# Performance work log

Measured on AMD Instinct MI355X. Metric: run time of the kernel, lower is better.

## Reference

```python
import jax, jax.numpy as jnp
import numpy as np

# CODABlocks (codomain attention) with per_channel_attention=True:
# token_codimension = head_codimension = 1, scale = 2, n_modes = [32, 32],
# mixer_modes = [16, 16], temperature = 1.0, instance_norm (affine) everywhere.
N_HEADS = 16
TEMPERATURE = 1.0
EPS = 1e-5

def _gelu(z):
    return jax.nn.gelu(z, approximate=False)  # matches torch F.gelu default (erf)

def instance_norm(x, g, b):
    # x: (B, C, H, W); normalize over spatial dims per (sample, channel), affine.
    mu = jnp.mean(x, axis=(-2, -1), keepdims=True)
    var = jnp.var(x, axis=(-2, -1), keepdims=True)
    return (x - mu) * jax.lax.rsqrt(var + EPS) * g[:, None, None] + b[:, None, None]

def conv1x1(x, w, b):
    return jnp.einsum('bihw,io->bohw', x, w) + b[None, :, None, None]

def fourier_resample(x, out_shape):
    # FFT-based spatial resampling (mode truncation / zero-pad), norm='forward'.
    if tuple(x.shape[-2:]) == tuple(out_shape):
        return x
    Ho, Wo = out_shape
    xft = jnp.fft.rfftn(x, axes=(-2, -1), norm='forward')
    out = jnp.zeros(x.shape[:-2] + (Ho, Wo // 2 + 1), dtype=xft.dtype)
    hk = min(x.shape[-2], Ho) // 2
    wk = min(xft.shape[-1], Wo // 2 + 1)
    out = out.at[..., :hk, :wk].set(xft[..., :hk, :wk])
    out = out.at[..., -hk:, :wk].set(xft[..., -hk:, :wk])
    return jnp.fft.irfftn(out, s=out_shape, axes=(-2, -1), norm='forward')

def spectral_conv(x, w, out_shape):
    # Truncated-mode spectral convolution (dense weights, equiv. to tucker rank=1.0).
    # w: (Cin, Cout, 2*mh, mw, 2) -> complex weight on kept Fourier modes.
    wc = w[..., 0] + 1j * w[..., 1]
    mh = wc.shape[2] // 2
    mw = wc.shape[3]
    Ho, Wo = out_shape
    xft = jnp.fft.rfftn(x, axes=(-2, -1), norm='forward')   # (B, Cin, H, W//2+1)
    top = jnp.einsum('bihw,iohw->bohw', xft[:, :, :mh, :mw], wc[:, :, :mh])
    bot = jnp.einsum('bihw,iohw->bohw', xft[:, :, -mh:, :mw], wc[:, :, mh:])
    out_ft = jnp.zeros((x.shape[0], wc.shape[1], Ho, Wo // 2 + 1), dtype=xft.dtype)
    out_ft = out_ft.at[:, :, :mh, :mw].set(top)
    out_ft = out_ft.at[:, :, -mh:, :mw].set(bot)
    return jnp.fft.irfftn(out_ft, s=out_shape, axes=(-2, -1), norm='forward')

def fno_layer(x, spec_w, skip_w, skip_b, out_shape, norm=None, act=None):
    # One FNOBlocks layer: spectral conv + (resampled) linear skip, optional norm/act.
    xs = fourier_resample(conv1x1(x, skip_w, skip_b), out_shape)
    xf = spectral_conv(x, spec_w, out_shape)
    if norm is not None:
        xf = instance_norm(xf, *norm)
    y = xf + xs
    return act(y) if act is not None else y

def codano_forward(x, key_w, key_skip_w, key_skip_b, query_w, query_skip_w, query_skip_b, value_w, value_skip_w, value_skip_b, proj_w, proj_skip_w, proj_skip_b, norm1_g, norm1_b, attn_norm_g, attn_norm_b, norm2_g, norm2_b, mixer_w1, mixer_skip_w1, mixer_skip_b1, mixer_norm_g1, mixer_norm_b1, mixer_w2, mixer_skip_w2, mixer_skip_b2, mixer_norm_g2, mixer_norm_b2, mixer_out_g, mixer_out_b):
    b, t, H, W = x.shape   # token codim d = 1 -> channel dim == number of tokens
    tokens = x.reshape(b * t, 1, H, W)
    tokens_norm = instance_norm(tokens, norm1_g, norm1_b)
    Hs, Ws = H // 2, W // 2   # K, Q downsampled by scale = 2
    k = fno_layer(tokens_norm, key_w, key_skip_w, key_skip_b, (Hs, Ws))
    q = fno_layer(tokens_norm, query_w, query_skip_w, query_skip_b, (Hs, Ws))
    v = fno_layer(tokens_norm, value_w, value_skip_w, value_skip_b, (H, W))

    def heads_flat(z):
        hh, ww = z.shape[-2:]
        # (b*t, n_heads*d, h, w) -> (b, heads, t, d*h*w), d = 1
        return z.reshape(b, t, N_HEADS, hh * ww).transpose(0, 2, 1, 3)

    kf, qf, vf = heads_flat(k), heads_flat(q), heads_flat(v)
    scale = jnp.sqrt(jnp.asarray(kf.shape[-1], jnp.float32)) * TEMPERATURE
    dprod = jax.nn.softmax(jnp.einsum('bhtd,bhsd->bhts', qf, kf) / scale, axis=-1)
    attn = jnp.einsum('bhts,bhsd->bhtd', dprod, vf)      # (b, heads, t, H*W)
    attn = attn.transpose(0, 2, 1, 3).reshape(b * t, N_HEADS, H, W)
    # multi-head projection back to token codimension (n_heads -> 1)
    attn = fno_layer(attn, proj_w, proj_skip_w, proj_skip_b, (H, W))
    attn = instance_norm(attn + tokens, attn_norm_g, attn_norm_b)
    # permutation-equivariant mixer: 2 FNO layers shared across all tokens
    m = instance_norm(attn, norm2_g, norm2_b)
    m = fno_layer(m, mixer_w1, mixer_skip_w1, mixer_skip_b1, (H, W), norm=(mixer_norm_g1, mixer_norm_b1), act=_gelu)
    m = fno_layer(m, mixer_w2, mixer_skip_w2, mixer_skip_b2, (H, W), norm=(mixer_norm_g2, mixer_norm_b2))
    out = instance_norm(m, mixer_out_g, mixer_out_b) + attn
    return out.reshape(b, t, H, W)

def setup_inputs():
    key = jax.random.key(0)
    ks = list(jax.random.split(key, 32))
    f32 = jnp.float32
    def W_(k, shape, s=0.02):
        return (s * jax.random.normal(k, shape)).astype(f32)
    B, T, H, Wd = 4, 32, 128, 128
    mh_s, mw_s = 16, 9    # mixer_modes [16,16]: 2*(16//2) rows, 16//2+1 rfft cols
    mh_f, mw_f = 32, 17   # n_modes [32,32]
    return {
        'x': jax.random.normal(ks[0], (B, T, H, Wd), dtype=f32),
        'key_w': W_(ks[1], (1, N_HEADS, mh_s, mw_s, 2)),
        'key_skip_w': W_(ks[2], (1, N_HEADS), 0.5),
        'key_skip_b': W_(ks[3], (N_HEADS,)),
        'query_w': W_(ks[4], (1, N_HEADS, mh_s, mw_s, 2)),
        'query_skip_w': W_(ks[5], (1, N_HEADS), 0.5),
        'query_skip_b': W_(ks[6], (N_HEADS,)),
        'value_w': W_(ks[7], (1, N_HEADS, mh_s, mw_s, 2)),
        'value_skip_w': W_(ks[8], (1, N_HEADS), 0.5),
        'value_skip_b': W_(ks[9], (N_HEADS,)),
        'proj_w': W_(ks[10], (N_HEADS, 1, mh_f, mw_f, 2)),
        'proj_skip_w': W_(ks[11], (N_HEADS, 1), 0.25),
        'proj_skip_b': W_(ks[12], (1,)),
        'norm1_g': jnp.ones((1,), f32), 'norm1_b': jnp.zeros((1,), f32),
        'attn_norm_g': jnp.ones((1,), f32), 'attn_norm_b': jnp.zeros((1,), f32),
        'norm2_g': jnp.ones((1,), f32), 'norm2_b': jnp.zeros((1,), f32),
        'mixer_w1': W_(ks[13], (1, 1, mh_f, mw_f, 2)),
        'mixer_skip_w1': W_(ks[14], (1, 1), 0.5),
        'mixer_skip_b1': W_(ks[15], (1,)),
        'mixer_norm_g1': jnp.ones((1,), f32), 'mixer_norm_b1': jnp.zeros((1,), f32),
        'mixer_w2': W_(ks[16], (1, 1, mh_f, mw_f, 2)),
        'mixer_skip_w2': W_(ks[17], (1, 1), 0.5),
        'mixer_skip_b2': W_(ks[18], (1,)),
        'mixer_norm_g2': jnp.ones((1,), f32), 'mixer_norm_b2': jnp.zeros((1,), f32),
        'mixer_out_g': jnp.ones((1,), f32), 'mixer_out_b': jnp.zeros((1,), f32),
    }

def reference(x, key_w, key_skip_w, key_skip_b, query_w, query_skip_w, query_skip_b, value_w, value_skip_w, value_skip_b, proj_w, proj_skip_w, proj_skip_b, norm1_g, norm1_b, attn_norm_g, attn_norm_b, norm2_g, norm2_b, mixer_w1, mixer_skip_w1, mixer_skip_b1, mixer_norm_g1, mixer_norm_b1, mixer_w2, mixer_skip_w2, mixer_skip_b2, mixer_norm_g2, mixer_norm_b2, mixer_out_g, mixer_out_b):
    return codano_forward(x, key_w, key_skip_w, key_skip_b, query_w, query_skip_w, query_skip_b, value_w, value_skip_w, value_skip_b, proj_w, proj_skip_w, proj_skip_b, norm1_g, norm1_b, attn_norm_g, attn_norm_b, norm2_g, norm2_b, mixer_w1, mixer_skip_w1, mixer_skip_b1, mixer_norm_g1, mixer_norm_b1, mixer_w2, mixer_skip_w2, mixer_skip_b2, mixer_norm_g2, mixer_norm_b2, mixer_out_g, mixer_out_b)
```

## Files before the change

### kernel.cpp

```cpp
#include <hip/hip_runtime.h>
#include <cmath>

#define PI_F 3.14159265358979323846f
#define NTOK 128
#define NPIX 16384
#define NHEADS 16

__device__ __forceinline__ void block_reduce2(float& a, float& b){
  __shared__ float sa[4], sb[4];
  __syncthreads();
  for (int o=32;o>0;o>>=1){ a += __shfl_down(a,o); b += __shfl_down(b,o); }
  int w = threadIdx.x>>6, l = threadIdx.x&63;
  if (l==0){ sa[w]=a; sb[w]=b; }
  __syncthreads();
  a = sa[0]+sa[1]+sa[2]+sa[3];
  b = sb[0]+sb[1]+sb[2]+sb[3];
}

__device__ __forceinline__ float block_reduce1(float a){
  __shared__ float sa[4];
  __syncthreads();
  for (int o=32;o>0;o>>=1) a += __shfl_down(a,o);
  int w = threadIdx.x>>6, l = threadIdx.x&63;
  if (l==0) sa[w]=a;
  __syncthreads();
  return sa[0]+sa[1]+sa[2]+sa[3];
}

__device__ __forceinline__ float gelu_f(float y){
  return 0.5f*y*(1.f + erff(y*0.70710678118f));
}

__device__ __forceinline__ void affine_from(const float* __restrict__ ps, float g, float bb, int t,
                                            float& a, float& b0){
  float sum=0.f,sq=0.f;
  #pragma unroll
  for (int s=0;s<8;s++){ const float* p=ps+((size_t)t*8+s)*2; sum+=p[0]; sq+=p[1]; }
  const float iN=1.f/NPIX;
  float mu=sum*iN, var=sq*iN-mu*mu;
  a=rsqrtf(var+1e-5f)*g;
  b0=bb-mu*a;
}
__device__ __forceinline__ void scalA_from(const float* __restrict__ psA, float ag, float n2g, int t,
                                           float& muZ, float& aA, float& a0){
  float sum=0.f,sq=0.f;
  #pragma unroll
  for (int s=0;s<16;s++){ const float* p=psA+((size_t)t*16+s)*2; sum+=p[0]; sq+=p[1]; }
  const float iN=1.f/NPIX;
  muZ=sum*iN; float var=sq*iN-muZ*muZ;
  float inv=rsqrtf(var+1e-5f);
  aA=inv*ag;
  float var2=aA*aA*var;
  a0=aA*rsqrtf(var2+1e-5f)*n2g;
}
__device__ __forceinline__ void scalB_from(const float* __restrict__ psB, float mng1, int t,
                                           float& mu1, float& c1){
  float sum=0.f,sq=0.f;
  #pragma unroll
  for (int s=0;s<16;s++){ const float* p=psB+((size_t)t*16+s)*2; sum+=p[0]; sq+=p[1]; }
  const float iN=1.f/NPIX;
  mu1=sum*iN; float var=sq*iN-mu1*mu1;
  c1=rsqrtf(var+1e-5f)*mng1;
}
__device__ __forceinline__ void scalC_from(const float* __restrict__ psC, float mng2, float K, float sw,
                                           float outg, int t,
                                           float& mu2f, float& c2, float& mu3, float& c3){
  float sf=0.f,sfsq=0.f,sm=0.f,smsq=0.f,sx=0.f;
  #pragma unroll
  for (int s=0;s<16;s++){
    const float* p=psC+((size_t)t*16+s)*5;
    sf+=p[0]; sfsq+=p[1]; sm+=p[2]; smsq+=p[3]; sx+=p[4];
  }
  const float iN=1.f/NPIX;
  mu2f=sf*iN; float var2=sfsq*iN-mu2f*mu2f;
  c2=rsqrtf(var2+1e-5f)*mng2;
  float Em1=sm*iN, Em1sq=smsq*iN, Exm=sx*iN;
  float Em2=K+sw*Em1;
  float Em2sq = c2*c2*var2 + sw*sw*Em1sq + K*K
              + 2.f*c2*sw*(Exm - mu2f*Em1) + 2.f*K*sw*Em1;
  float var_m2=Em2sq-Em2*Em2;
  mu3=Em2;
  c3=rsqrtf(var_m2+1e-5f)*outg;
}

__global__ __launch_bounds__(256) void k_stats0(const float* __restrict__ x, float* __restrict__ pstat){
  int t=blockIdx.x, slab=blockIdx.y;
  const float* xs = x + (size_t)t*NPIX + slab*2048;
  float sum=0.f, sq=0.f;
  for (int i=threadIdx.x;i<2048;i+=256){ float v=xs[i]; sum+=v; sq+=v*v; }
  block_reduce2(sum,sq);
  if (threadIdx.x==0){ float* o=pstat+((size_t)t*8+slab)*2; o[0]=sum; o[1]=sq; }
}

__global__ __launch_bounds__(256) void k_colfft33(const float* __restrict__ x, const float* __restrict__ pstat0,
                          const float* __restrict__ n1g, const float* __restrict__ n1b,
                          float* __restrict__ A){
  __shared__ float rows[16*128];
  __shared__ float tw[128][2];
  int base = blockIdx.x*16;
  int t = base>>7;
  float a,b0; affine_from(pstat0, n1g[0], n1b[0], t, a, b0);
  for (int i=threadIdx.x;i<2048;i+=256) rows[i] = a*x[(size_t)base*128 + i] + b0;
  for (int p=threadIdx.x;p<128;p+=256){ float sn,cs; sincosf(-(2.f*PI_F/128.f)*(float)p,&sn,&cs); tw[p][0]=cs; tw[p][1]=sn; }
  __syncthreads();
  for (int e=threadIdx.x;e<16*33;e+=256){
    int r=e/33, c=e%33;
    const float* rp=rows+r*128;
    float re=0.f, im=0.f;
    for (int w=0;w<128;w++){
      int p=(c*w)&127;
      float v=rp[w];
      re+=v*tw[p][0]; im+=v*tw[p][1];
    }
    float* o=A+((size_t)(base+r)*33+c)*2; o[0]=re; o[1]=im;
  }
}

__global__ __launch_bounds__(256) void k_rowfft64(const float* __restrict__ A,
                          float* __restrict__ X64, float* __restrict__ X64h){
  int s=blockIdx.x, cg=blockIdx.y;
  int c0=cg*11;
  __shared__ float a[128][11][2];
  __shared__ float S[64][11][2];
  __shared__ float tw[128][2];
  for (int i=threadIdx.x;i<128*22;i+=256){
    int r=i/22, q=i%22;
    a[r][q>>1][q&1] = A[((size_t)(s*128+r)*33 + c0)*2 + q];
  }
  for (int p=threadIdx.x;p<128;p+=256){ float sn,cs; sincosf(-(2.f*PI_F/128.f)*(float)p,&sn,&cs); tw[p][0]=cs; tw[p][1]=sn; }
  __syncthreads();
  const float sc=1.f/16384.f;
  for (int e=threadIdx.x;e<64*11;e+=256){
    int i2=e/11, cl=e%11;
    int r=(i2<32)? i2 : i2+64;
    float re=0.f, im=0.f;
    for (int h=0;h<128;h++){
      int p=(r*h)&127;
      float cs=tw[p][0], sn=tw[p][1];
      float ar=a[h][cl][0], ai=a[h][cl][1];
      re+=ar*cs-ai*sn; im+=ar*sn+ai*cs;
    }
    S[i2][cl][0]=re*sc; S[i2][cl][1]=im*sc;
  }
  __syncthreads();
  for (int e=threadIdx.x;e<64*11;e+=256){
    int r=e/11, cl=e%11; int c=c0+cl;
    float vr=S[r][cl][0], vi=S[r][cl][1];
    float* o=X64+((size_t)s*(64*33)+r*33+c)*2; o[0]=vr; o[1]=vi;
    float hr=vr, hi=vi;
    if (c==0 || c==32){
      int pr=(64-r)&63;
      hr=0.5f*(vr+S[pr][cl][0]);
      hi=0.5f*(vi-S[pr][cl][1]);
    }
    float* oh=X64h+((size_t)s*(64*33)+r*33+c)*2; oh[0]=hr; oh[1]=hi;
  }
}

__global__ __launch_bounds__(256) void k_UeZYw(const float* __restrict__ X64, const float* __restrict__ X64h,
    const float* __restrict__ qw, const float* __restrict__ qsw,
    const float* __restrict__ kw, const float* __restrict__ ksw,
    const float* __restrict__ value_w, const float* __restrict__ vsw, const float* __restrict__ vsb,
    const float* __restrict__ proj_w, const float* __restrict__ psw,
    float* __restrict__ Zq, float* __restrict__ Zk, float* __restrict__ Yw,
    float* __restrict__ Ue){
  __shared__ float sh[4224];
  int bx=blockIdx.x;
  if (bx<2048){
    int t=bx>>4, h=bx&15;
    float* Xs = sh;
    float2* xh0 = (float2*)(sh+1092);
    for (int e=threadIdx.x;e<544;e+=256){
      int j=e/17, c=e%17;
      int i2=(j<16)? j : (j+32);
      const float* xp = X64 + ((size_t)t*(64*33) + i2*33 + c)*2;
      Xs[e*2]=xp[0]; Xs[e*2+1]=xp[1];
    }
    if (threadIdx.x<17){
      int j=threadIdx.x;
      int r=(j<=8)? j : j+47;
      const float* hp = X64h + ((size_t)t*(64*33) + r*33)*2;
      xh0[j]=make_float2(hp[0],hp[1]);
    }
    __syncthreads();
    float aq=qsw[h], ak=ksw[h];
    for (int e=threadIdx.x;e<306;e+=256){
      int side=e/153, m=e%153;
      int j=m/9, c=m%9;
      int jj=(j<=8)? j : j+15;
      const float* W = side? kw : qw;
      float a = side? ak : aq;
      float prx=0.f, pry=0.f;
      if (j!=8){
        int jw=(j<8)? j : j-1;
        const float* wp = W + ((size_t)(h*16+jw)*9 + c)*2;
        float xrr=Xs[(jj*17+c)*2], xri=Xs[(jj*17+c)*2+1];
        prx = wp[0]*xrr - wp[1]*xri;
        pry = wp[0]*xri + wp[1]*xrr;
      }
      float Vx=prx, Vy=pry;
      if (c==0){
        int jp = (j==0)? 0 : 17-j;
        float ppx=0.f, ppy=0.f;
        if (jp!=8){
// ... 137 lines not shown
    int e0=ec*64, hs0=g*128;
    float (*Pl)[32] = (float(*)[32])sh;
    for (int i=threadIdx.x;i<128*32;i+=256){
      int hsl=i>>5, t=i&31;
      int hs=hs0+hsl, h=hs>>5, s=hs&31;
      Pl[hsl][t]=P[(((size_t)(b*16+h)*32)+t)*32+s];
    }
    __syncthreads();
    int el=threadIdx.x&63, tg=threadIdx.x>>6;
    float acc[8];
    #pragma unroll
    for (int j=0;j<8;j++) acc[j]=0.f;
    const float* Yb = Yw + ((size_t)b*512 + hs0)*1088 + e0 + el;
    #pragma unroll 4
    for (int hsl=0;hsl<128;hsl++){
      float y = Yb[(size_t)hsl*1088];
      #pragma unroll
      for (int j=0;j<8;j++) acc[j] += Pl[hsl][tg*8+j]*y;
    }
    #pragma unroll
    for (int j=0;j<8;j++){
      int t=tg*8+j;
      Sfp[((size_t)(b*32+t)*4+g)*1088 + e0 + el] = acc[j];
    }
  } else {
    int u=bx-272;
    int b=u>>6, rem=u&63, ch=rem>>1, tt=rem&1;
    int pxb=ch*512;
    float* Rs = sh;
    float* cbs = sh+512;
    float* as2 = sh+528;
    float* b0s = sh+560;
    if (threadIdx.x<32){
      float a,b0; affine_from(pstat0, n1g[0], n1b[0], b*32+threadIdx.x, a, b0);
      as2[threadIdx.x]=a; b0s[threadIdx.x]=b0;
    }
    __syncthreads();
    for (int rr=threadIdx.x; rr<512; rr+=256){
      int tl=rr>>5, s=rr&31;
      int t=tt*16+tl;
      float acc=0.f;
      for (int h=0;h<16;h++)
        acc += pw[h]*vw[h]*P[(((size_t)(b*16+h)*32)+t)*32+s];
      Rs[tl*32+s]=acc*as2[s];
      float cb=acc*b0s[s];
      for (int o=16;o>0;o>>=1) cb+=__shfl_down(cb,o,32);
      if (s==0) cbs[tl]=cb;
    }
    __syncthreads();
    float a0[16], a1[16];
    #pragma unroll
    for (int t=0;t<16;t++){ a0[t]=0.f; a1[t]=0.f; }
    for (int s=0;s<32;s++){
      const float* xp = x + ((size_t)(b*32+s))*NPIX + pxb;
      float v0=xp[threadIdx.x], v1=xp[threadIdx.x+256];
      #pragma unroll
      for (int t=0;t<16;t++){ float r=Rs[t*32+s]; a0[t]+=r*v0; a1[t]+=r*v1; }
    }
    #pragma unroll
    for (int t=0;t<16;t++){
      int gt=tt*16+t;
      float cb=cbs[t];
      float* op = sk + ((size_t)(b*32+gt))*NPIX + pxb;
      op[threadIdx.x]=a0[t]+cb; op[threadIdx.x+256]=a1[t]+cb;
    }
  }
}

__global__ __launch_bounds__(256) void k_field0(const float* __restrict__ Sfp,
        const float* __restrict__ sk, const float* __restrict__ x,
        const float* __restrict__ psw, const float* __restrict__ vsb, const float* __restrict__ psb,
        float* __restrict__ zf, float* __restrict__ pstatA){
  int bt = blockIdx.x, slab = blockIdx.y;
  __shared__ float Ss[1088];
  __shared__ float T[8*17*2];
  __shared__ float tw[128][2];
  for (int i=threadIdx.x;i<1088;i+=256){
    const float* sp4 = Sfp + (size_t)bt*4352 + i;
    Ss[i] = sp4[0]+sp4[1088]+sp4[2176]+sp4[3264];
  }
  for (int p=threadIdx.x;p<128;p+=256){ float sn,cs; sincosf((2.f*PI_F/128.f)*(float)p,&sn,&cs); tw[p][0]=cs; tw[p][1]=sn; }
  __syncthreads();
  int h0 = slab*8;
  for (int e=threadIdx.x;e<8*17;e+=256){
    int hl=e/17, c=e%17; int h=h0+hl;
    float re=0.f, im=0.f;
    for (int j=0;j<32;j++){
      int r=(j<16)? j : (j+96);
      int p=(r*h)&127;
      float cs=tw[p][0], sn=tw[p][1];
      float ar=Ss[(j*17+c)*2], ai=Ss[(j*17+c)*2+1];
      re += ar*cs - ai*sn;
      im += ar*sn + ai*cs;
    }
    T[e*2]=re; T[e*2+1]=im;
  }
  __syncthreads();
  size_t base = (size_t)bt*NPIX + h0*128;
  float Cb = psb[0];
  for (int hh=0;hh<16;hh++) Cb += psw[hh]*vsb[hh];
  float sum=0.f, sq=0.f;
  for (int pos=threadIdx.x;pos<1024;pos+=256){
    int hl=pos>>7, w=pos&127;
    const float* Th=T+hl*17*2;
    float br=tw[w][0], bi=tw[w][1];
    float rr=br, ri=bi;
    float v=Th[0];
    for (int c=1;c<17;c++){
      v += 2.f*(Th[c*2]*rr - Th[c*2+1]*ri);
      float nr=rr*br-ri*bi; ri=rr*bi+ri*br; rr=nr;
    }
    float val = v + sk[base+pos] + x[base+pos] + Cb;
    zf[base+pos]=val; sum+=val; sq+=val*val;
  }
  block_reduce2(sum,sq);
  if (threadIdx.x==0){ float* o=pstatA+((size_t)bt*16+slab)*2; o[0]=sum; o[1]=sq; }
}

__global__ __launch_bounds__(256) void k_specm0(const float* __restrict__ P,
    const float* __restrict__ pw, const float* __restrict__ vw,
    const float* __restrict__ Sfp, const float* __restrict__ X64,
    const float* __restrict__ pstat0, const float* __restrict__ pstatA,
    const float* __restrict__ n1g, const float* __restrict__ n1b,
    const float* __restrict__ ag, const float* __restrict__ n2g, const float* __restrict__ n2b,
    const float* __restrict__ psw, const float* __restrict__ vsb, const float* __restrict__ psb,
    float* __restrict__ sp){
  int bt=blockIdx.x, ec=blockIdx.y; int b=bt>>5, t=bt&31;
  __shared__ float Rs[32];
  __shared__ float Sfl[1088];
  if (threadIdx.x<32){
    int s=threadIdx.x; float acc=0.f;
    for (int h=0;h<16;h++)
      acc += pw[h]*vw[h]*P[(((size_t)(b*16+h)*32)+t)*32+s];
    Rs[s]=acc;
  }
  for (int i=threadIdx.x;i<1088;i+=256){
    const float* sp4 = Sfp + (size_t)bt*4352 + i;
    Sfl[i]=sp4[0]+sp4[1088]+sp4[2176]+sp4[3264];
  }
  __syncthreads();
  float a_t,b0_t; affine_from(pstat0,n1g[0],n1b[0],bt,a_t,b0_t);
  float muZ,aA,a0; scalA_from(pstatA,ag[0],n2g[0],bt,muZ,aA,a0);
  float Cb=psb[0];
  for (int h=0;h<16;h++) Cb+=psw[h]*vsb[h];
  float inva=1.f/a_t;
  int e1=ec*272, e2=e1+272;
  for (int e=e1+threadIdx.x;e<e2;e+=256){
    int j=e/17, c=e%17;
    float sr=Sfl[e*2], si=Sfl[e*2+1];
    if (c==0){
      if (j==0){ si=0.f; }
      else if (j==16){ sr*=0.5f; si*=0.5f; }
      else { int jp=32-j; sr=0.5f*(sr+Sfl[jp*34]); si=0.5f*(si-Sfl[jp*34+1]); }
    }
    int i2=(j<16)? j : (j+32);
    float re=0.f, im=0.f;
    const float* xb = X64 + ((size_t)(b*32)*(64*33) + i2*33 + c)*2;
    for (int s=0;s<32;s++){
      const float* xp = xb + (size_t)s*(64*33)*2;
      float r=Rs[s];
      re += r*xp[0]; im += r*xp[1];
    }
    const float* xt = X64 + ((size_t)bt*(64*33) + i2*33 + c)*2;
    re += inva*xt[0]; im += inva*xt[1];
    float zr=sr+re, zi=si+im;
    if (e==0) zr += Cb - b0_t*inva;
    float mr=a0*zr, mi=a0*zi;
    if (e==0) mr += n2b[0] - muZ*a0;
    sp[((size_t)bt*544+e)*2]=mr; sp[((size_t)bt*544+e)*2+1]=mi;
  }
}

__global__ __launch_bounds__(256) void k_field1(const float* __restrict__ sp, const float* __restrict__ wm,
        float* __restrict__ fd1, float* __restrict__ pstatB){
  int bt = blockIdx.x, slab = blockIdx.y;
  __shared__ float Ss[1088];
  __shared__ float T[8*17*2];
  __shared__ float tw[128][2];
  for (int e=threadIdx.x;e<544;e+=256){
    float xr=sp[((size_t)bt*544+e)*2], xi=sp[((size_t)bt*544+e)*2+1];
    float wr=wm[e*2], wi=wm[e*2+1];
    Ss[e*2]=xr*wr-xi*wi; Ss[e*2+1]=xr*wi+xi*wr;
  }
  for (int p=threadIdx.x;p<128;p+=256){ float sn,cs; sincosf((2.f*PI_F/128.f)*(float)p,&sn,&cs); tw[p][0]=cs; tw[p][1]=sn; }
  __syncthreads();
  int h0 = slab*8;
  for (int e=threadIdx.x;e<8*17;e+=256){
    int hl=e/17, c=e%17; int h=h0+hl;
    float re=0.f, im=0.f;
    for (int j=0;j<32;j++){
      int r=(j<16)? j : (j+96);
      int p=(r*h)&127;
      float cs=tw[p][0], sn=tw[p][1];
      float ar=Ss[(j*17+c)*2], ai=Ss[(j*17+c)*2+1];
      re += ar*cs - ai*sn;
      im += ar*sn + ai*cs;
    }
    T[e*2]=re; T[e*2+1]=im;
  }
  __syncthreads();
  size_t base = (size_t)bt*NPIX + h0*128;
  float sum=0.f, sq=0.f;
  for (int pos=threadIdx.x;pos<1024;pos+=256){
    int hl=pos>>7, w=pos&127;
    const float* Th=T+hl*17*2;
    float br=tw[w][0], bi=tw[w][1];
    float rr=br, ri=bi;
    float v=Th[0];
    for (int c=1;c<17;c++){
      v += 2.f*(Th[c*2]*rr - Th[c*2+1]*ri);
      float nr=rr*br-ri*bi; ri=rr*bi+ri*br; rr=nr;
    }
    fd1[base+pos]=v; sum+=v; sq+=v*v;
  }
  block_reduce2(sum,sq);
  if (threadIdx.x==0){ float* o=pstatB+((size_t)bt*16+slab)*2; o[0]=sum; o[1]=sq; }
}

__global__ __launch_bounds__(256) void k_colA1(const float* __restrict__ f1, const float* __restrict__ z,
        const float* __restrict__ pstatA, const float* __restrict__ pstatB,
        const float* __restrict__ ag, const float* __restrict__ n2g, const float* __restrict__ mng1,
        const float* __restrict__ n2b,
        const float* __restrict__ mnb1, const float* __restrict__ msw1, const float* __restrict__ msb1,
        float* __restrict__ A){
  __shared__ float rows[16*128];
  __shared__ float tw[128][2];
  int grow = blockIdx.x*16;
  int t = grow>>7;
  float muZ,aA,a0;
  scalA_from(pstatA, ag[0], n2g[0], t, muZ, aA, a0);
  float b2 = n2b[0];
  float mu1,c1;
  scalB_from(pstatB, mng1[0], t, mu1, c1);
  float nb=mnb1[0], sw=msw1[0], sb=msb1[0];
  for (int i=threadIdx.x;i<2048;i+=256){
    size_t gi=(size_t)grow*128+i;
    float m0v=(z[gi]-muZ)*a0+b2;
    float y=(f1[gi]-mu1)*c1+nb + m0v*sw + sb;
    rows[i]=gelu_f(y);
  }
  for (int p=threadIdx.x;p<128;p+=256){ float sn,cs; sincosf(-(2.f*PI_F/128.f)*(float)p,&sn,&cs); tw[p][0]=cs; tw[p][1]=sn; }
  __syncthreads();
  for (int e=threadIdx.x;e<16*17;e+=256){
    int r=e/17, c=e%17;
    const float* rp=rows+r*128;
    float re=0.f, im=0.f;
    for (int w=0;w<128;w++){
      int p=(c*w)&127;
      float v=rp[w];
      re+=v*tw[p][0]; im+=v*tw[p][1];
    }
    float* o=A+((size_t)(grow+r)*17+c)*2; o[0]=re; o[1]=im;
  }
}

__global__ __launch_bounds__(256) void k_rowfft32(const float* __restrict__ A, float* __restrict__ spec){
  int s=blockIdx.x, cg=blockIdx.y;
  int c0 = (cg==0)? 0 : (1+cg*4);
  int nc = (cg==0)? 5 : 4;
  __shared__ float a[128*5*2];
  __shared__ float tw[128][2];
  for (int i=threadIdx.x;i<128*nc*2;i+=256){
    int r=i/(2*nc), q=i%(2*nc);
    a[(r*5+(q>>1))*2+(q&1)] = A[((size_t)(s*128+r)*17 + c0)*2 + q];
  }
  for (int p=threadIdx.x;p<128;p+=256){ float sn,cs; sincosf(-(2.f*PI_F/128.f)*(float)p,&sn,&cs); tw[p][0]=cs; tw[p][1]=sn; }
  __syncthreads();
  const float sc=1.f/16384.f;
  for (int e=threadIdx.x;e<32*nc;e+=256){
    int j=e/nc, cl=e%nc;
    int r=(j<16)? j : (j+96);
    float re=0.f,im=0.f;
    for (int h=0;h<128;h++){
      int p=(r*h)&127;
      float cs=tw[p][0], sn=tw[p][1];
      float ar=a[(h*5+cl)*2], ai=a[(h*5+cl)*2+1];
      re += ar*cs - ai*sn;
      im += ar*sn + ai*cs;
    }
    float* o=spec+((size_t)s*544 + j*17 + c0+cl)*2;
    o[0]=re*sc; o[1]=im*sc;
  }
}

__global__ __launch_bounds__(256) void k_field2(const float* __restrict__ sp2, const float* __restrict__ wm,
        const float* __restrict__ f1, const float* __restrict__ z,
        const float* __restrict__ pstatA, const float* __restrict__ pstatB,
        const float* __restrict__ ag, const float* __restrict__ n2g, const float* __restrict__ mng1,
        const float* __restrict__ n2b, const float* __restrict__ mnb1,
        const float* __restrict__ msw1, const float* __restrict__ msb1,
        float* __restrict__ fd2, float* __restrict__ pstatC){
  int bt = blockIdx.x, slab = blockIdx.y;
  __shared__ float Ss[1088];
  __shared__ float T[8*17*2];
  __shared__ float tw[128][2];
  for (int e=threadIdx.x;e<544;e+=256){
    float xr=sp2[((size_t)bt*544+e)*2], xi=sp2[((size_t)bt*544+e)*2+1];
    float wr=wm[e*2], wi=wm[e*2+1];
    Ss[e*2]=xr*wr-xi*wi; Ss[e*2+1]=xr*wi+xi*wr;
  }
  for (int p=threadIdx.x;p<128;p+=256){ float sn,cs; sincosf((2.f*PI_F/128.f)*(float)p,&sn,&cs); tw[p][0]=cs; tw[p][1]=sn; }
  __syncthreads();
  int h0 = slab*8;
  for (int e=threadIdx.x;e<8*17;e+=256){
    int hl=e/17, c=e%17; int h=h0+hl;
    float re=0.f, im=0.f;
    for (int j=0;j<32;j++){
      int r=(j<16)? j : (j+96);
      int p=(r*h)&127;
      float cs=tw[p][0], sn=tw[p][1];
      float ar=Ss[(j*17+c)*2], ai=Ss[(j*17+c)*2+1];
      re += ar*cs - ai*sn;
      im += ar*sn + ai*cs;
    }
    T[e*2]=re; T[e*2+1]=im;
  }
  __syncthreads();
  size_t base = (size_t)bt*NPIX + h0*128;
  float muZ,aA,a0,mu1,c1;
  scalA_from(pstatA, ag[0], n2g[0], bt, muZ, aA, a0);
  scalB_from(pstatB, mng1[0], bt, mu1, c1);
  float b2=n2b[0], nb1=mnb1[0], sw1=msw1[0], sb1=msb1[0];
  float s_f=0.f,s_fsq=0.f,s_m=0.f,s_msq=0.f,s_x=0.f;
  for (int pos=threadIdx.x;pos<1024;pos+=256){
    int hl=pos>>7, w=pos&127;
    const float* Th=T+hl*17*2;
    float br=tw[w][0], bi=tw[w][1];
    float rr=br, ri=bi;
    float v=Th[0];
    for (int c=1;c<17;c++){
      v += 2.f*(Th[c*2]*rr - Th[c*2+1]*ri);
      float nr=rr*br-ri*bi; ri=rr*bi+ri*br; rr=nr;
    }
    size_t gi=base+pos;
    float m0v=(z[gi]-muZ)*a0+b2;
    float y=(f1[gi]-mu1)*c1+nb1 + m0v*sw1 + sb1;
    float m1v=gelu_f(y);
    fd2[gi]=v;
    s_f+=v; s_fsq+=v*v; s_m+=m1v; s_msq+=m1v*m1v; s_x+=v*m1v;
  }
  block_reduce2(s_f,s_fsq);
  block_reduce2(s_m,s_msq);
  s_x = block_reduce1(s_x);
  if (threadIdx.x==0){
    float* o=pstatC+((size_t)bt*16+slab)*5;
    o[0]=s_f; o[1]=s_fsq; o[2]=s_m; o[3]=s_msq; o[4]=s_x;
  }
}

__global__ __launch_bounds__(256) void k_final2(const float* __restrict__ z, const float* __restrict__ f1,
        const float* __restrict__ f2,
        const float* __restrict__ pstatA, const float* __restrict__ pstatB, const float* __restrict__ pstatC,
        const float* __restrict__ ag, const float* __restrict__ n2g, const float* __restrict__ mng1,
        const float* __restrict__ mng2, const float* __restrict__ outg,
        const float* __restrict__ ab, const float* __restrict__ n2b,
        const float* __restrict__ mnb1, const float* __restrict__ msw1, const float* __restrict__ msb1,
        const float* __restrict__ mnb2, const float* __restrict__ msw2, const float* __restrict__ msb2,
        const float* __restrict__ outb, float* __restrict__ out){
  int bt=blockIdx.x, slab=blockIdx.y;
  float muZ,aA,a0,mu1,c1,mu2f,c2,mu3,c3;
  scalA_from(pstatA, ag[0], n2g[0], bt, muZ, aA, a0);
  scalB_from(pstatB, mng1[0], bt, mu1, c1);
  float sw2=msw2[0], K=mnb2[0]+msb2[0];
  scalC_from(pstatC, mng2[0], K, sw2, outg[0], bt, mu2f, c2, mu3, c3);
  float b1=ab[0], b2=n2b[0], nb1=mnb1[0], sw1=msw1[0], sb1=msb1[0];
  float nb2=mnb2[0], sb2=msb2[0], bo=outb[0];
  size_t base=(size_t)bt*NPIX + (size_t)slab*1024;
  for (int i=threadIdx.x;i<1024;i+=256){
    size_t gi=base+i;
    float zv=z[gi];
    float m0v=(zv-muZ)*a0+b2;
    float a2v=(zv-muZ)*aA+b1;
    float y=(f1[gi]-mu1)*c1+nb1 + m0v*sw1 + sb1;
    float m1v=gelu_f(y);
    float m2v=(f2[gi]-mu2f)*c2+nb2 + m1v*sw2 + sb2;
    out[gi]=(m2v-mu3)*c3+bo+a2v;
  }
}

extern "C" void kernel_launch(void* const* d_in, const int* in_sizes, int n_in,
                              void* d_out, int out_size, void* d_ws, size_t ws_size,
                              hipStream_t stream){
  const float* x        = (const float*)d_in[0];
  const float* key_w    = (const float*)d_in[1];
  const float* key_sw   = (const float*)d_in[2];
  const float* key_sb   = (const float*)d_in[3];
  const float* query_w  = (const float*)d_in[4];
  const float* query_sw = (const float*)d_in[5];
  const float* query_sb = (const float*)d_in[6];
  const float* value_w  = (const float*)d_in[7];
  const float* value_sw = (const float*)d_in[8];
  const float* value_sb = (const float*)d_in[9];
  const float* proj_w   = (const float*)d_in[10];
  const float* proj_sw  = (const float*)d_in[11];
  const float* proj_sb  = (const float*)d_in[12];
  const float* norm1_g  = (const float*)d_in[13];
  const float* norm1_b  = (const float*)d_in[14];
  const float* attn_g   = (const float*)d_in[15];
  const float* attn_b   = (const float*)d_in[16];
  const float* norm2_g  = (const float*)d_in[17];
  const float* norm2_b  = (const float*)d_in[18];
  const float* mw1      = (const float*)d_in[19];
  const float* msw1     = (const float*)d_in[20];
  const float* msb1     = (const float*)d_in[21];
  const float* mng1     = (const float*)d_in[22];
  const float* mnb1     = (const float*)d_in[23];
  const float* mw2      = (const float*)d_in[24];
  const float* msw2     = (const float*)d_in[25];
  const float* msb2     = (const float*)d_in[26];
  const float* mng2     = (const float*)d_in[27];
  const float* mnb2     = (const float*)d_in[28];
  const float* outg     = (const float*)d_in[29];
  const float* outb     = (const float*)d_in[30];
  float* out = (float*)d_out;
  float* ws  = (float*)d_ws;

  size_t off=0;
  float* A   = ws + off; off += (size_t)128*128*33*2;
  float* X64 = ws + off; off += (size_t)128*64*33*2;
  float* X64h= ws + off; off += (size_t)128*64*33*2;
  float* Zq  = ws + off; off += (size_t)128*16*306;
  float* Zk  = ws + off; off += (size_t)128*16*306;
  float* Ue  = ws + off; off += (size_t)4*32*32;
  float* P   = ws + off; off += (size_t)4*16*32*32;
  float* Yw  = ws + off; off += (size_t)2048*1088;
  float* Sfp = ws + off; off += (size_t)128*4*1088;
  float* sk  = ws + off; off += (size_t)128*16384;
  float* zf  = ws + off; off += (size_t)128*16384;
  float* fd1 = ws + off; off += (size_t)128*16384;
  float* fd2 = ws + off; off += (size_t)128*16384;
  float* sp  = ws + off; off += (size_t)128*544*2;
  float* sp2 = ws + off; off += (size_t)128*544*2;
  float* pstat0 = ws + off; off += (size_t)128*8*2;
  float* pstatA = ws + off; off += (size_t)128*16*2;
  float* pstatB = ws + off; off += (size_t)128*16*2;
  float* pstatC = ws + off; off += (size_t)128*16*5;

  k_stats0<<<dim3(128,8),256,0,stream>>>(x, pstat0);
  k_colfft33<<<1024,256,0,stream>>>(x, pstat0, norm1_g, norm1_b, A);
  k_rowfft64<<<dim3(128,3),256,0,stream>>>(A, X64, X64h);
  k_UeZYw<<<3072,256,0,stream>>>(X64, X64h, query_w, query_sw, key_w, key_sw,
      value_w, value_sw, value_sb, proj_w, proj_sw, Zq, Zk, Yw, Ue);
  k_scores2<<<dim3(4,16,2),256,0,stream>>>(Zq, Zk, Ue, query_sw, query_sb, key_sw, key_sb, P);
  k_SfSk<<<528,256,0,stream>>>(x, P, Yw, proj_sw, value_sw, pstat0, norm1_g, norm1_b, Sfp, sk);

  k_field0<<<dim3(128,16),256,0,stream>>>(Sfp, sk, x, proj_sw, value_sb, proj_sb, zf, pstatA);
  k_specm0<<<dim3(128,2),256,0,stream>>>(P, proj_sw, value_sw, Sfp, X64, pstat0, pstatA,
      norm1_g, norm1_b, attn_g, norm2_g, norm2_b, proj_sw, value_sb, proj_sb, sp);
  k_field1<<<dim3(128,16),256,0,stream>>>(sp, mw1, fd1, pstatB);
  k_colA1<<<1024,256,0,stream>>>(fd1, zf, pstatA, pstatB, attn_g, norm2_g, mng1,
      norm2_b, mnb1, msw1, msb1, A);
  k_rowfft32<<<dim3(128,4),256,0,stream>>>(A, sp2);
  k_field2<<<dim3(128,16),256,0,stream>>>(sp2, mw2, fd1, zf, pstatA, pstatB,
      attn_g, norm2_g, mng1, norm2_b, mnb1, msw1, msb1, fd2, pstatC);
  k_final2<<<dim3(128,16),256,0,stream>>>(zf, fd1, fd2, pstatA, pstatB, pstatC,
      attn_g, norm2_g, mng1, mng2, outg, attn_b, norm2_b,
      mnb1, msw1, msb1, mnb2, msw2, msb2, outb, out);
}
```

Baseline: 307.6 us.

## Fuse tail kernel chain into one cooperative persistent kernel with grid syncs

Replaces the seven tail launches (field0, specm0, field1, colA1, rowfft32, field2, final2) with one cooperative kernel of 512 blocks that loops over the same work units and separates the stages with grid-wide syncs. The aim is to remove per-launch overhead and the gaps between dependent small kernels. In exchange it adds grid barrier cost, caps parallelism at the resident grid, and falls back to the separate launches if the cooperative launch fails.

```diff
diff --git a/kernel.cpp b/kernel.cpp
--- a/kernel.cpp
+++ b/kernel.cpp
@@ -1,5 +1,8 @@
 #include <hip/hip_runtime.h>
+#include <hip/hip_cooperative_groups.h>
 #include <cmath>
+
+namespace cg = cooperative_groups;
 
 #define PI_F 3.14159265358979323846f
 #define NTOK 128
@@ -118,8 +121,8 @@
 
 __global__ __launch_bounds__(256) void k_rowfft64(const float* __restrict__ A,
                           float* __restrict__ X64, float* __restrict__ X64h){
-  int s=blockIdx.x, cg=blockIdx.y;
-  int c0=cg*11;
+  int s=blockIdx.x, cg2=blockIdx.y;
+  int c0=cg2*11;
   __shared__ float a[128][11][2];
   __shared__ float S[64][11][2];
   __shared__ float tw[128][2];
@@ -423,7 +426,7 @@
   for (int p=threadIdx.x;p<128;p+=256){ float sn,cs; sincosf((2.f*PI_F/128.f)*(float)p,&sn,&cs); tw[p][0]=cs; tw[p][1]=sn; }
   __syncthreads();
   int h0 = slab*8;
-  for (int e=threadIdx.x;e<8*17;e+=256){
+  for (int e=threadIdx.x;e<136;e+=256){
     int hl=e/17, c=e%17; int h=h0+hl;
     float re=0.f, im=0.f;
     for (int j=0;j<32;j++){
@@ -526,7 +529,7 @@
   for (int p=threadIdx.x;p<128;p+=256){ float sn,cs; sincosf((2.f*PI_F/128.f)*(float)p,&sn,&cs); tw[p][0]=cs; tw[p][1]=sn; }
   __syncthreads();
   int h0 = slab*8;
-  for (int e=threadIdx.x;e<8*17;e+=256){
+  for (int e=threadIdx.x;e<136;e+=256){
     int hl=e/17, c=e%17; int h=h0+hl;
     float re=0.f, im=0.f;
     for (int j=0;j<32;j++){
@@ -596,9 +599,9 @@
 }
 
 __global__ __launch_bounds__(256) void k_rowfft32(const float* __restrict__ A, float* __restrict__ spec){
-  int s=blockIdx.x, cg=blockIdx.y;
-  int c0 = (cg==0)? 0 : (1+cg*4);
-  int nc = (cg==0)? 5 : 4;
+  int s=blockIdx.x, cg2=blockIdx.y;
+  int c0 = (cg2==0)? 0 : (1+cg2*4);
+  int nc = (cg2==0)? 5 : 4;
   __shared__ float a[128*5*2];
   __shared__ float tw[128][2];
   for (int i=threadIdx.x;i<128*nc*2;i+=256){
@@ -643,7 +646,7 @@
   for (int p=threadIdx.x;p<128;p+=256){ float sn,cs; sincosf((2.f*PI_F/128.f)*(float)p,&sn,&cs); tw[p][0]=cs; tw[p][1]=sn; }
   __syncthreads();
   int h0 = slab*8;
-  for (int e=threadIdx.x;e<8*17;e+=256){
+  for (int e=threadIdx.x;e<136;e+=256){
     int hl=e/17, c=e%17; int h=h0+hl;
     float re=0.f, im=0.f;
     for (int j=0;j<32;j++){
@@ -716,6 +719,322 @@
     float m1v=gelu_f(y);
     float m2v=(f2[gi]-mu2f)*c2+nb2 + m1v*sw2 + sb2;
     out[gi]=(m2v-mu3)*c3+bo+a2v;
+  }
+}
+
+struct TailArgs {
+  const float *Sfp, *sk, *x, *P, *X64, *pstat0;
+  float *pstatA, *pstatB, *pstatC, *sp, *sp2, *A, *zf, *fd1, *fd2, *out;
+  const float *n1g,*n1b,*ag,*n2g,*n2b,*mng1,*mnb1,*msw1,*msb1,*mw1,*mw2;
+  const float *mng2,*mnb2,*msw2,*msb2,*outg,*outb,*ab,*psw,*vsb,*psb,*pw,*vw;
+};
+
+#define TAIL_GRID 512
+
+__global__ __launch_bounds__(256,2) void k_tail(TailArgs Aa){
+  cg::grid_group gg = cg::this_grid();
+  __shared__ float sh[2304];
+
+  {
+    float* tw = sh+1360;
+    for (int p=threadIdx.x;p<128;p+=256){ float sn,cs; sincosf((2.f*PI_F/128.f)*(float)p,&sn,&cs); tw[p*2]=cs; tw[p*2+1]=sn; }
+    float Cb = Aa.psb[0];
+    for (int hh=0;hh<16;hh++) Cb += Aa.psw[hh]*Aa.vsb[hh];
+    for (int u=blockIdx.x; u<2048; u+=TAIL_GRID){
+      int bt=u>>4, slab=u&15;
+      __syncthreads();
+      float* Ss=sh; float* T=sh+1088;
+      for (int i=threadIdx.x;i<1088;i+=256){
+        const float* sp4 = Aa.Sfp + (size_t)bt*4352 + i;
+        Ss[i] = sp4[0]+sp4[1088]+sp4[2176]+sp4[3264];
+      }
+      __syncthreads();
+      int h0 = slab*8;
+      for (int e=threadIdx.x;e<136;e+=256){
+        int hl=e/17, c=e%17; int h=h0+hl;
+        float re=0.f, im=0.f;
+        for (int j=0;j<32;j++){
+          int r=(j<16)? j : (j+96);
+          int p=(r*h)&127;
+          float cs=tw[p*2], sn=tw[p*2+1];
+          float ar=Ss[(j*17+c)*2], ai=Ss[(j*17+c)*2+1];
+          re += ar*cs - ai*sn;
+          im += ar*sn + ai*cs;
+        }
+        T[e*2]=re; T[e*2+1]=im;
+      }
+      __syncthreads();
+      size_t base = (size_t)bt*NPIX + h0*128;
+      float sum=0.f, sq=0.f;
+      for (int pos=threadIdx.x;pos<1024;pos+=256){
+        int hl=pos>>7, w=pos&127;
+        const float* Th=T+hl*17*2;
+        float br=tw[w*2], bi=tw[w*2+1];
+        float rr=br, ri=bi;
+        float v=Th[0];
+        for (int c=1;c<17;c++){
+          v += 2.f*(Th[c*2]*rr - Th[c*2+1]*ri);
+          float nr=rr*br-ri*bi; ri=rr*bi+ri*br; rr=nr;
+        }
+        float val = v + Aa.sk[base+pos] + Aa.x[base+pos] + Cb;
+        Aa.zf[base+pos]=val; sum+=val; sq+=val*val;
+      }
+      block_reduce2(sum,sq);
+      if (threadIdx.x==0){ float* o=Aa.pstatA+((size_t)bt*16+slab)*2; o[0]=sum; o[1]=sq; }
+    }
+  }
+  gg.sync();
+
+  {
+    for (int u=blockIdx.x; u<256; u+=TAIL_GRID){
+      int bt=u>>1, ec=u&1; int b=bt>>5, t=bt&31;
+      __syncthreads();
+      float* Sfl=sh; float* Rs=sh+1088;
+      if (threadIdx.x<32){
+        int s=threadIdx.x; float acc=0.f;
+        for (int h=0;h<16;h++)
+          acc += Aa.pw[h]*Aa.vw[h]*Aa.P[(((size_t)(b*16+h)*32)+t)*32+s];
+        Rs[s]=acc;
+      }
+      for (int i=threadIdx.x;i<1088;i+=256){
+        const float* sp4 = Aa.Sfp + (size_t)bt*4352 + i;
+        Sfl[i]=sp4[0]+sp4[1088]+sp4[2176]+sp4[3264];
+      }
+      __syncthreads();
+      float a_t,b0_t; affine_from(Aa.pstat0,Aa.n1g[0],Aa.n1b[0],bt,a_t,b0_t);
+      float muZ,aA,a0; scalA_from(Aa.pstatA,Aa.ag[0],Aa.n2g[0],bt,muZ,aA,a0);
+      float Cb=Aa.psb[0];
+      for (int h=0;h<16;h++) Cb+=Aa.psw[h]*Aa.vsb[h];
+      float inva=1.f/a_t;
+      int e1=ec*272, e2=e1+272;
+      for (int e=e1+threadIdx.x;e<e2;e+=256){
+        int j=e/17, c=e%17;
+        float sr=Sfl[e*2], si=Sfl[e*2+1];
+        if (c==0){
+          if (j==0){ si=0.f; }
+          else if (j==16){ sr*=0.5f; si*=0.5f; }
+          else { int jp=32-j; sr=0.5f*(sr+Sfl[jp*34]); si=0.5f*(si-Sfl[jp*34+1]); }
+        }
+        int i2=(j<16)? j : (j+32);
+        float re=0.f, im=0.f;
+        const float* xb = Aa.X64 + ((size_t)(b*32)*(64*33) + i2*33 + c)*2;
+        for (int s=0;s<32;s++){
+          const float* xp = xb + (size_t)s*(64*33)*2;
+          float r=Rs[s];
+          re += r*xp[0]; im += r*xp[1];
+        }
+        const float* xt = Aa.X64 + ((size_t)bt*(64*33) + i2*33 + c)*2;
+        re += inva*xt[0]; im += inva*xt[1];
+        float zr=sr+re, zi=si+im;
+        if (e==0) zr += Cb - b0_t*inva;
+        float mr=a0*zr, mi=a0*zi;
+        if (e==0) mr += Aa.n2b[0] - muZ*a0;
+        Aa.sp[((size_t)bt*544+e)*2]=mr; Aa.sp[((size_t)bt*544+e)*2+1]=mi;
+      }
+    }
+  }
+  gg.sync();
+
+  {
+    float* tw = sh+1360;
+    for (int p=threadIdx.x;p<128;p+=256){ float sn,cs; sincosf((2.f*PI_F/128.f)*(float)p,&sn,&cs); tw[p*2]=cs; tw[p*2+1]=sn; }
+    for (int u=blockIdx.x; u<2048; u+=TAIL_GRID){
+      int bt=u>>4, slab=u&15;
+      __syncthreads();
+      float* Ss=sh; float* T=sh+1088;
+      for (int e=threadIdx.x;e<544;e+=256){
+        float xr=Aa.sp[((size_t)bt*544+e)*2], xi=Aa.sp[((size_t)bt*544+e)*2+1];
+        float wr=Aa.mw1[e*2], wi=Aa.mw1[e*2+1];
+        Ss[e*2]=xr*wr-xi*wi; Ss[e*2+1]=xr*wi+xi*wr;
+      }
+      __syncthreads();
+      int h0 = slab*8;
+      for (int e=threadIdx.x;e<136;e+=256){
+        int hl=e/17, c=e%17; int h=h0+hl;
+        float re=0.f, im=0.f;
+        for (int j=0;j<32;j++){
+          int r=(j<16)? j : (j+96);
+          int p=(r*h)&127;
+          float cs=tw[p*2], sn=tw[p*2+1];
+          float ar=Ss[(j*17+c)*2], ai=Ss[(j*17+c)*2+1];
+          re += ar*cs - ai*sn;
+          im += ar*sn + ai*cs;
+        }
+        T[e*2]=re; T[e*2+1]=im;
+      }
+      __syncthreads();
+      size_t base = (size_t)bt*NPIX + h0*128;
+      float sum=0.f, sq=0.f;
+      for (int pos=threadIdx.x;pos<1024;pos+=256){
+        int hl=pos>>7, w=pos&127;
+        const float* Th=T+hl*17*2;
+        float br=tw[w*2], bi=tw[w*2+1];
+        float rr=br, ri=bi;
+        float v=Th[0];
+        for (int c=1;c<17;c++){
+          v += 2.f*(Th[c*2]*rr - Th[c*2+1]*ri);
+          float nr=rr*br-ri*bi; ri=rr*bi+ri*br; rr=nr;
+        }
+        Aa.fd1[base+pos]=v; sum+=v; sq+=v*v;
+      }
+      block_reduce2(sum,sq);
+      if (threadIdx.x==0){ float* o=Aa.pstatB+((size_t)bt*16+slab)*2; o[0]=sum; o[1]=sq; }
+    }
+  }
+  gg.sync();
+
+  {
+    float* tw = sh+2048;
+    for (int p=threadIdx.x;p<128;p+=256){ float sn,cs; sincosf(-(2.f*PI_F/128.f)*(float)p,&sn,&cs); tw[p*2]=cs; tw[p*2+1]=sn; }
+    for (int u=blockIdx.x; u<1024; u+=TAIL_GRID){
+      int grow=u*16; int t=grow>>7;
+      __syncthreads();
+      float* rows=sh;
+      float muZ,aA,a0;
+      scalA_from(Aa.pstatA, Aa.ag[0], Aa.n2g[0], t, muZ, aA, a0);
+      float b2 = Aa.n2b[0];
+      float mu1,c1;
+      scalB_from(Aa.pstatB, Aa.mng1[0], t, mu1, c1);
+      float nb=Aa.mnb1[0], sw=Aa.msw1[0], sb=Aa.msb1[0];
+      for (int i=threadIdx.x;i<2048;i+=256){
+        size_t gi=(size_t)grow*128+i;
+        float m0v=(Aa.zf[gi]-muZ)*a0+b2;
+        float y=(Aa.fd1[gi]-mu1)*c1+nb + m0v*sw + sb;
+        rows[i]=gelu_f(y);
+      }
+      __syncthreads();
+      for (int e=threadIdx.x;e<16*17;e+=256){
+        int r=e/17, c=e%17;
+        const float* rp=rows+r*128;
+        float re=0.f, im=0.f;
+        for (int w=0;w<128;w++){
+          int p=(c*w)&127;
+          float v=rp[w];
+          re+=v*tw[p*2]; im+=v*tw[p*2+1];
+        }
+        float* o=Aa.A+((size_t)(grow+r)*17+c)*2; o[0]=re; o[1]=im;
+      }
+    }
+  }
+  gg.sync();
+
+  {
+    float* tw = sh+2048;
+    for (int p=threadIdx.x;p<128;p+=256){ float sn,cs; sincosf(-(2.f*PI_F/128.f)*(float)p,&sn,&cs); tw[p*2]=cs; tw[p*2+1]=sn; }
+    const float sc=1.f/16384.f;
+    for (int u=blockIdx.x; u<512; u+=TAIL_GRID){
+      int s=u>>2, cg2=u&3;
+      int c0 = (cg2==0)? 0 : (1+cg2*4);
+      int nc = (cg2==0)? 5 : 4;
+      __syncthreads();
+      float* a=sh;
+      for (int i=threadIdx.x;i<128*nc*2;i+=256){
+        int r=i/(2*nc), q=i%(2*nc);
+        a[(r*5+(q>>1))*2+(q&1)] = Aa.A[((size_t)(s*128+r)*17 + c0)*2 + q];
+      }
+      __syncthreads();
+      for (int e=threadIdx.x;e<32*nc;e+=256){
+        int j=e/nc, cl=e%nc;
+        int r=(j<16)? j : (j+96);
+        float re=0.f,im=0.f;
+        for (int h=0;h<128;h++){
+          int p=(r*h)&127;
+          float cs=tw[p*2], sn=tw[p*2+1];
+          float ar=a[(h*5+cl)*2], ai=a[(h*5+cl)*2+1];
+          re += ar*cs - ai*sn;
+          im += ar*sn + ai*cs;
+        }
+        float* o=Aa.sp2+((size_t)s*544 + j*17 + c0+cl)*2;
+        o[0]=re*sc; o[1]=im*sc;
+      }
+    }
+  }
+  gg.sync();
+
+  {
+    float* tw = sh+1360;
+    for (int p=threadIdx.x;p<128;p+=256){ float sn,cs; sincosf((2.f*PI_F/128.f)*(float)p,&sn,&cs); tw[p*2]=cs; tw[p*2+1]=sn; }
+    for (int u=blockIdx.x; u<2048; u+=TAIL_GRID){
+      int bt=u>>4, slab=u&15;
+      __syncthreads();
+      float* Ss=sh; float* T=sh+1088;
+      for (int e=threadIdx.x;e<544;e+=256){
+        float xr=Aa.sp2[((size_t)bt*544+e)*2], xi=Aa.sp2[((size_t)bt*544+e)*2+1];
+        float wr=Aa.mw2[e*2], wi=Aa.mw2[e*2+1];
+        Ss[e*2]=xr*wr-xi*wi; Ss[e*2+1]=xr*wi+xi*wr;
+      }
+      __syncthreads();
+      int h0 = slab*8;
+      for (int e=threadIdx.x;e<136;e+=256){
+        int hl=e/17, c=e%17; int h=h0+hl;
+        float re=0.f, im=0.f;
+        for (int j=0;j<32;j++){
+          int r=(j<16)? j : (j+96);
+          int p=(r*h)&127;
+          float cs=tw[p*2], sn=tw[p*2+1];
+          float ar=Ss[(j*17+c)*2], ai=Ss[(j*17+c)*2+1];
+          re += ar*cs - ai*sn;
+          im += ar*sn + ai*cs;
+        }
+        T[e*2]=re; T[e*2+1]=im;
+      }
+      __syncthreads();
+      size_t base = (size_t)bt*NPIX + h0*128;
+      float muZ,aA,a0,mu1,c1;
+      scalA_from(Aa.pstatA, Aa.ag[0], Aa.n2g[0], bt, muZ, aA, a0);
+      scalB_from(Aa.pstatB, Aa.mng1[0], bt, mu1, c1);
+      float b2=Aa.n2b[0], nb1=Aa.mnb1[0], sw1=Aa.msw1[0], sb1=Aa.msb1[0];
+      float s_f=0.f,s_fsq=0.f,s_m=0.f,s_msq=0.f,s_x=0.f;
+      for (int pos=threadIdx.x;pos<1024;pos+=256){
+        int hl=pos>>7, w=pos&127;
+        const float* Th=T+hl*17*2;
+        float br=tw[w*2], bi=tw[w*2+1];
+        float rr=br, ri=bi;
+        float v=Th[0];
+        for (int c=1;c<17;c++){
+          v += 2.f*(Th[c*2]*rr - Th[c*2+1]*ri);
+          float nr=rr*br-ri*bi; ri=rr*bi+ri*br; rr=nr;
+        }
+        size_t gi=base+pos;
+        float m0v=(Aa.zf[gi]-muZ)*a0+b2;
+        float y=(Aa.fd1[gi]-mu1)*c1+nb1 + m0v*sw1 + sb1;
+        float m1v=gelu_f(y);
+        Aa.fd2[gi]=v;
+        s_f+=v; s_fsq+=v*v; s_m+=m1v; s_msq+=m1v*m1v; s_x+=v*m1v;
+      }
+      block_reduce2(s_f,s_fsq);
+      block_reduce2(s_m,s_msq);
+      s_x = block_reduce1(s_x);
+      if (threadIdx.x==0){
+        float* o=Aa.pstatC+((size_t)bt*16+slab)*5;
+        o[0]=s_f; o[1]=s_fsq; o[2]=s_m; o[3]=s_msq; o[4]=s_x;
+      }
+    }
+  }
+  gg.sync();
+
+  {
+    for (int u=blockIdx.x; u<2048; u+=TAIL_GRID){
+      int bt=u>>4, slab=u&15;
+      float muZ,aA,a0,mu1,c1,mu2f,c2,mu3,c3;
+      scalA_from(Aa.pstatA, Aa.ag[0], Aa.n2g[0], bt, muZ, aA, a0);
+      scalB_from(Aa.pstatB, Aa.mng1[0], bt, mu1, c1);
+      float sw2=Aa.msw2[0], K=Aa.mnb2[0]+Aa.msb2[0];
+      scalC_from(Aa.pstatC, Aa.mng2[0], K, sw2, Aa.outg[0], bt, mu2f, c2, mu3, c3);
+      float b1=Aa.ab[0], b2=Aa.n2b[0], nb1=Aa.mnb1[0], sw1=Aa.msw1[0], sb1=Aa.msb1[0];
+      float nb2=Aa.mnb2[0], sb2=Aa.msb2[0], bo=Aa.outb[0];
+      size_t base=(size_t)bt*NPIX + (size_t)slab*1024;
+      for (int i=threadIdx.x;i<1024;i+=256){
+        size_t gi=base+i;
+        float zv=Aa.zf[gi];
+        float m0v=(zv-muZ)*a0+b2;
+        float a2v=(zv-muZ)*aA+b1;
+        float y=(Aa.fd1[gi]-mu1)*c1+nb1 + m0v*sw1 + sb1;
+        float m1v=gelu_f(y);
+        float m2v=(Aa.fd2[gi]-mu2f)*c2+nb2 + m1v*sw2 + sb2;
+        Aa.out[gi]=(m2v-mu3)*c3+bo+a2v;
+      }
+    }
   }
 }
 
@@ -785,16 +1104,30 @@
   k_scores2<<<dim3(4,16,2),256,0,stream>>>(Zq, Zk, Ue, query_sw, query_sb, key_sw, key_sb, P);
   k_SfSk<<<528,256,0,stream>>>(x, P, Yw, proj_sw, value_sw, pstat0, norm1_g, norm1_b, Sfp, sk);
 
-  k_field0<<<dim3(128,16),256,0,stream>>>(Sfp, sk, x, proj_sw, value_sb, proj_sb, zf, pstatA);
-  k_specm0<<<dim3(128,2),256,0,stream>>>(P, proj_sw, value_sw, Sfp, X64, pstat0, pstatA,
-      norm1_g, norm1_b, attn_g, norm2_g, norm2_b, proj_sw, value_sb, proj_sb, sp);
-  k_field1<<<dim3(128,16),256,0,stream>>>(sp, mw1, fd1, pstatB);
-  k_colA1<<<1024,256,0,stream>>>(fd1, zf, pstatA, pstatB, attn_g, norm2_g, mng1,
-      norm2_b, mnb1, msw1, msb1, A);
-  k_rowfft32<<<dim3(128,4),256,0,stream>>>(A, sp2);
-  k_field2<<<dim3(128,16),256,0,stream>>>(sp2, mw2, fd1, zf, pstatA, pstatB,
-      attn_g, norm2_g, mng1, norm2_b, mnb1, msw1, msb1, fd2, pstatC);
-  k_final2<<<dim3(128,16),256,0,stream>>>(zf, fd1, fd2, pstatA, pstatB, pstatC,
-      attn_g, norm2_g, mng1, mng2, outg, attn_b, norm2_b,
-      mnb1, msw1, msb1, mnb2, msw2, msb2, outb, out);
-}
+  TailArgs ta;
+  ta.Sfp=Sfp; ta.sk=sk; ta.x=x; ta.P=P; ta.X64=X64; ta.pstat0=pstat0;
+  ta.pstatA=pstatA; ta.pstatB=pstatB; ta.pstatC=pstatC; ta.sp=sp; ta.sp2=sp2;
+  ta.A=A; ta.zf=zf; ta.fd1=fd1; ta.fd2=fd2; ta.out=out;
+  ta.n1g=norm1_g; ta.n1b=norm1_b; ta.ag=attn_g; ta.n2g=norm2_g; ta.n2b=norm2_b;
+  ta.mng1=mng1; ta.mnb1=mnb1; ta.msw1=msw1; ta.msb1=msb1; ta.mw1=mw1; ta.mw2=mw2;
+  ta.mng2=mng2; ta.mnb2=mnb2; ta.msw2=msw2; ta.msb2=msb2; ta.outg=outg; ta.outb=outb;
+  ta.ab=attn_b; ta.psw=proj_sw; ta.vsb=value_sb; ta.psb=proj_sb; ta.pw=proj_sw; ta.vw=value_sw;
+  void* kargs[] = { &ta };
+  hipError_t cerr = hipLaunchCooperativeKernel((const void*)k_tail, dim3(TAIL_GRID), dim3(256),
+                                               kargs, 0, stream);
+  if (cerr != hipSuccess){
+    (void)hipGetLastError();
+    k_field0<<<dim3(128,16),256,0,stream>>>(Sfp, sk, x, proj_sw, value_sb, proj_sb, zf, pstatA);
+    k_specm0<<<dim3(128,2),256,0,stream>>>(P, proj_sw, value_sw, Sfp, X64, pstat0, pstatA,
+        norm1_g, norm1_b, attn_g, norm2_g, norm2_b, proj_sw, value_sb, proj_sb, sp);
+    k_field1<<<dim3(128,16),256,0,stream>>>(sp, mw1, fd1, pstatB);
+    k_colA1<<<1024,256,0,stream>>>(fd1, zf, pstatA, pstatB, attn_g, norm2_g, mng1,
+        norm2_b, mnb1, msw1, msb1, A);
+    k_rowfft32<<<dim3(128,4),256,0,stream>>>(A, sp2);
+    k_field2<<<dim3(128,16),256,0,stream>>>(sp2, mw2, fd1, zf, pstatA, pstatB,
+        attn_g, norm2_g, mng1, norm2_b, mnb1, msw1, msb1, fd2, pstatC);
+    k_final2<<<dim3(128,16),256,0,stream>>>(zf, fd1, fd2, pstatA, pstatB, pstatC,
+        attn_g, norm2_g, mng1, mng2, outg, attn_b, norm2_b,
+        mnb1, msw1, msb1, mnb2, msw2, msb2, outb, out);
+  }
+}
```

After: 664.2 us. +115.9%, slower.
